# Performance work log

Hardware: AMD Instinct MI355X
Metric: run time of the kernel (lower is better)

The kernel has to match this reference:

```python
import jax, jax.numpy as jnp
import numpy as np

B = 16384
D_VIS, D_LANG, D_STATE = 768, 768, 64
D = 256          # d_model
E = 4            # n_experts
K = 2            # top_k
D_IN = D_VIS + D_LANG + D_STATE
EPS = 1e-5


def layernorm(x, g, b):
    mu = x.mean(-1, keepdims=True)
    var = ((x - mu) ** 2).mean(-1, keepdims=True)
    return g * (x - mu) / jnp.sqrt(var + EPS) + b


def setup_inputs() -> dict:
    key = jax.random.key(0)
    ks = jax.random.split(key, 16)
    s = 0.02
    return {
        "vis": jax.random.normal(ks[0], (B, D_VIS), jnp.float32),
        "lang": jax.random.normal(ks[1], (B, D_LANG), jnp.float32),
        "state": jax.random.normal(ks[2], (B, D_STATE), jnp.float32),
        # fusion: Linear(d_in, d_model) + LayerNorm
        "Wf": jax.random.normal(ks[3], (D_IN, D), jnp.float32) * s,
        "bf": jnp.zeros((D,), jnp.float32),
        "gf": jnp.ones((D,), jnp.float32),
        "bfln": jnp.zeros((D,), jnp.float32),
        # gate (bias=False); random instead of zeros so routing is nontrivial
        "Wg": jax.random.normal(ks[4], (D, E), jnp.float32) * s,
        # stacked experts: Linear(d,2d) -> GELU -> Linear(2d,d) -> GELU -> Linear(d,d), then LN(x + net(x))
        "W1": jax.random.normal(ks[5], (E, D, 2 * D), jnp.float32) * s,
        "b1": jnp.zeros((E, 2 * D), jnp.float32),
        "W2": jax.random.normal(ks[6], (E, 2 * D, D), jnp.float32) * s,
        "b2": jnp.zeros((E, D), jnp.float32),
        "W3": jax.random.normal(ks[7], (E, D, D), jnp.float32) * s,
        "b3": jnp.zeros((E, D), jnp.float32),
        "eg": jnp.ones((E, D), jnp.float32),
        "eb": jnp.zeros((E, D), jnp.float32),
    }


def reference(vis, lang, state, Wf, bf, gf, bfln, Wg, W1, b1, W2, b2, W3, b3, eg, eb):
    gelu = lambda t: jax.nn.gelu(t, approximate=False)
    # fusion: Linear -> LayerNorm -> GELU  (dropout is eval-mode identity)
    x = jnp.concatenate([vis, lang, state], axis=-1) @ Wf + bf   # [B, D]
    x = gelu(layernorm(x, gf, bfln))

    logits = x @ Wg                                              # [B, E]
    all_probs = jax.nn.softmax(logits, axis=-1)
    top_vals, top_idx = jax.lax.top_k(logits, K)                 # [B, K]
    top_w = jax.nn.softmax(top_vals, axis=-1)                    # [B, K]

    # all experts densely (E small); original computes same math per masked subset
    h = gelu(jnp.einsum('bd,edh->beh', x, W1) + b1)              # [B, E, 2D]
    h = gelu(jnp.einsum('beh,ehd->bed', h, W2) + b2)             # [B, E, D]
    h = jnp.einsum('bed,edf->bef', h, W3) + b3                   # [B, E, D]
    y = layernorm(x[:, None, :] + h, eg, eb)                     # [B, E, D]

    # gather selected experts and combine with top-k weights
    y_sel = jnp.take_along_axis(y, top_idx[:, :, None], axis=1)  # [B, K, D]
    out = jnp.einsum('bk,bkd->bd', top_w, y_sel)                 # [B, D]

    # load-balance loss: importance x load
    counts = jnp.zeros((E,), x.dtype).at[top_idx.reshape(-1)].add(1.0)
    f_i = counts / (B * K)
    lb_loss = E * jnp.sum(f_i * all_probs.mean(0))
    return out, lb_loss
```

## Files before the change

### kernel.cpp

```cpp
#include <hip/hip_runtime.h>
#include <math.h>


typedef unsigned short u16;
typedef unsigned int u32;
typedef __attribute__((ext_vector_type(8))) short bf16x8;
typedef __attribute__((ext_vector_type(4))) float f32x4;

__device__ __forceinline__ float bf2f(u16 u) {
    union { u32 i; float f; } v; v.i = ((u32)u) << 16; return v.f;
}
__device__ __forceinline__ u16 f2bf(float f) {
    union { float f; u32 i; } v; v.f = f;
    u32 x = v.i;
    return (u16)((x + 0x7fffu + ((x >> 16) & 1u)) >> 16);
}
__device__ __forceinline__ float gelu_exact(float v) {
    return 0.5f * v * (1.0f + erff(v * 0.70710678118654752f));
}

typedef __attribute__((address_space(1))) void GV;
typedef __attribute__((address_space(3))) void SV;
__device__ __forceinline__ void gldlds(const void* g, void* l) {
    __builtin_amdgcn_global_load_lds((GV*)g, (SV*)l, 16, 0, 0);
}

__device__ __forceinline__ u32 pk2(u32 f0, u32 f1) {
    return __builtin_amdgcn_perm(f1, f0, 0x07060302);
}

__device__ __forceinline__ void stageA64(const u16* Ag, int lda, u16* As, int tid) {
#pragma unroll
    for (int i = 0; i < 2; ++i) {
        int s = i * 256 + tid;
        int m = s >> 3, c = s & 7;
        gldlds(Ag + m * lda + (c ^ (m & 7)) * 8, As + s * 8);
    }
}
__device__ __forceinline__ void stageA64_R32(const u16* Ag, int lda, u16* As, int tid) {
    int s = tid;
    int m = s >> 3, c = s & 7;
    gldlds(Ag + m * lda + (c ^ (m & 7)) * 8, As + s * 8);
}
__device__ __forceinline__ void stageB64(const u16* Bg, int ldb, u16* Bs, int tid) {
#pragma unroll
    for (int i = 0; i < 8; ++i) {
        int s = i * 256 + tid;
        int n = s >> 3, c = s & 7;
        gldlds(Bg + n * ldb + (c ^ (n & 7)) * 8, Bs + s * 8);
    }
}
__device__ __forceinline__ void compute64(const u16* As, const u16* Bs, f32x4 acc[4][4],
                                          int w, int l16, int quad) {
#pragma unroll
    for (int ks = 0; ks < 2; ++ks) {
        bf16x8 a[4];
#pragma unroll
        for (int mt = 0; mt < 4; ++mt) {
            int m = mt * 16 + l16;
            a[mt] = *(const bf16x8*)(As + m * 64 + (((ks * 4 + quad) ^ (m & 7)) << 3));
        }
#pragma unroll
        for (int nt = 0; nt < 4; ++nt) {
            int n = w * 64 + nt * 16 + l16;
            bf16x8 b = *(const bf16x8*)(Bs + n * 64 + (((ks * 4 + quad) ^ (n & 7)) << 3));
#pragma unroll
            for (int mt = 0; mt < 4; ++mt)
                acc[mt][nt] = __builtin_amdgcn_mfma_f32_16x16x32_bf16(a[mt], b, acc[mt][nt], 0, 0, 0);
        }
    }
}
__device__ __forceinline__ void compute64_R32(const u16* As, const u16* Bs, f32x4 acc[2][4],
                                              int w, int l16, int quad) {
#pragma unroll
    for (int ks = 0; ks < 2; ++ks) {
        bf16x8 a[2];
#pragma unroll
        for (int mt = 0; mt < 2; ++mt) {
            int m = mt * 16 + l16;
            a[mt] = *(const bf16x8*)(As + m * 64 + (((ks * 4 + quad) ^ (m & 7)) << 3));
        }
#pragma unroll
        for (int nt = 0; nt < 4; ++nt) {
            int n = w * 64 + nt * 16 + l16;
            bf16x8 b = *(const bf16x8*)(Bs + n * 64 + (((ks * 4 + quad) ^ (n & 7)) << 3));
#pragma unroll
            for (int mt = 0; mt < 2; ++mt)
                acc[mt][nt] = __builtin_amdgcn_mfma_f32_16x16x32_bf16(a[mt], b, acc[mt][nt], 0, 0, 0);
        }
    }
}

#define SEG_WF  409600
#define SEG_W1  524288
#define SEG_W2  524288
#define SEG_W3  262144
#define PREP_ITEMS (SEG_WF + SEG_W1 + SEG_W2 + SEG_W3 + 8)

__global__ __launch_bounds__(256) void prep_kernel(
    const float* __restrict__ Wf, const float* __restrict__ W1, const float* __restrict__ W2,
    const float* __restrict__ W3,
    u16* __restrict__ wft, u16* __restrict__ w1t, u16* __restrict__ w2t, u16* __restrict__ w3t,
    float* __restrict__ lbacc) {
    int idx = blockIdx.x * 256 + threadIdx.x;
    if (idx < SEG_WF) {
        int n = idx / 1600, k = idx % 1600;
        wft[idx] = f2bf(Wf[(size_t)k * 256 + n]);
        return;
    }
    idx -= SEG_WF;
    if (idx < SEG_W1) {
        int e = idx >> 17, r = idx & 131071;
        int n = r >> 8, k = r & 255;
        w1t[idx] = f2bf(W1[(size_t)e * 131072 + (size_t)k * 512 + n]);
        return;
    }
    idx -= SEG_W1;
    if (idx < SEG_W2) {
        int e = idx >> 17, r = idx & 131071;
        int n = r >> 9, k = r & 511;
        w2t[idx] = f2bf(W2[(size_t)e * 131072 + (size_t)k * 256 + n]);
        return;
    }
    idx -= SEG_W2;
    if (idx < SEG_W3) {
        int e = idx >> 16, r = idx & 65535;
        int n = r >> 8, k = r & 255;
        w3t[idx] = f2bf(W3[(size_t)e * 65536 + (size_t)k * 256 + n]);
        return;
    }
    idx -= SEG_W3;
    if (idx < 8) lbacc[idx] = 0.0f;
}

__global__ __launch_bounds__(256) void fusion_kernel(
    const float* __restrict__ vis, const float* __restrict__ lang, const float* __restrict__ state,
    const u16* __restrict__ BT, const float* __restrict__ bfv_, const float* __restrict__ gf,
    const float* __restrict__ bfln, const float* __restrict__ Wg,
    u16* __restrict__ xbf, float* __restrict__ wr, float* __restrict__ lbacc) {
    __shared__ __align__(16) u32 Af[2048];
    __shared__ __align__(16) u16 Bs[16384];
    int tid = threadIdx.x;
    int w = tid >> 6, lane = tid & 63, quad = lane >> 4, l16 = lane & 15;
    int m0 = blockIdx.x * 32;
    f32x4 acc[2][4] = {};

    for (int kit = 0; kit < 25; ++kit) {
        const float* base; int ld;
        if (kit < 12)      { base = vis   + (size_t)m0 * 768 + kit * 64;        ld = 768; }
        else if (kit < 24) { base = lang  + (size_t)m0 * 768 + (kit - 12) * 64; ld = 768; }
        else               { base = state + (size_t)m0 * 64;                    ld = 64; }
#pragma unroll
        for (int i = 0; i < 2; ++i) {
            int s = i * 256 + tid;
            int m = s >> 4, c = s & 15;
            gldlds(base + m * ld + (c ^ (m & 15)) * 4, Af + s * 4);
        }
        stageB64(BT + kit * 64, 1600, Bs, tid);
        __syncthreads();
#pragma unroll
        for (int ks = 0; ks < 2; ++ks) {
            bf16x8 a[2];
#pragma unroll
            for (int mt = 0; mt < 2; ++mt) {
                int m = mt * 16 + l16;
                int c0 = ks * 8 + quad * 2;
                const u32* rowp = Af + m * 64;
                uint4 f0 = *(const uint4*)(rowp + (c0 ^ (m & 15)) * 4);
                uint4 f1 = *(const uint4*)(rowp + ((c0 + 1) ^ (m & 15)) * 4);
                union { u32 u[4]; bf16x8 v; } pk;
                pk.u[0] = pk2(f0.x, f0.y); pk.u[1] = pk2(f0.z, f0.w);
                pk.u[2] = pk2(f1.x, f1.y); pk.u[3] = pk2(f1.z, f1.w);
                a[mt] = pk.v;
            }
#pragma unroll
            for (int nt = 0; nt < 4; ++nt) {
                int n = w * 64 + nt * 16 + l16;
                bf16x8 b = *(const bf16x8*)(Bs + n * 64 + (((ks * 4 + quad) ^ (n & 7)) << 3));
#pragma unroll
                for (int mt = 0; mt < 2; ++mt)
                    acc[mt][nt] = __builtin_amdgcn_mfma_f32_16x16x32_bf16(a[mt], b, acc[mt][nt], 0, 0, 0);
            }
        }
        __syncthreads();
    }

    float2* red  = (float2*)Af;
    float*  muv  = (float*)(Af + 256);
    float*  rsv  = (float*)(Af + 288);
    float*  gred = (float*)(Af + 512);
    float*  sacc = (float*)(Af + 1024);

    float bv[4], gvv[4], blv[4]; float4 wgv[4];
#pragma unroll
    for (int nt = 0; nt < 4; ++nt) {
        int col = w * 64 + nt * 16 + l16;
        bv[nt] = bfv_[col]; gvv[nt] = gf[col]; blv[nt] = bfln[col];
        wgv[nt] = *(const float4*)(Wg + col * 4);
    }
    if (tid < 8) sacc[tid] = 0.f;
#pragma unroll
    for (int mt = 0; mt < 2; ++mt)
#pragma unroll
        for (int r = 0; r < 4; ++r) {
            float ss = 0.f, qq = 0.f;
#pragma unroll
            for (int nt = 0; nt < 4; ++nt) {
                float v = acc[mt][nt][r] + bv[nt];
                acc[mt][nt][r] = v;
                ss += v; qq += v * v;
            }
#pragma unroll
            for (int d = 1; d < 16; d <<= 1) { ss += __shfl_xor(ss, d); qq += __shfl_xor(qq, d); }
            if (l16 == 0) red[w * 32 + mt * 16 + quad * 4 + r] = make_float2(ss, qq);
        }
    __syncthreads();
    if (tid < 32) {
        float ss = 0.f, qq = 0.f;
#pragma unroll
        for (int ww = 0; ww < 4; ++ww) { float2 t = red[ww * 32 + tid]; ss += t.x; qq += t.y; }
        float mu = ss * (1.f / 256.f);
        float var = qq * (1.f / 256.f) - mu * mu;
        muv[tid] = mu;
        rsv[tid] = 1.f / sqrtf(var + 1e-5f);
    }
    __syncthreads();
#pragma unroll
    for (int mt = 0; mt < 2; ++mt)
#pragma unroll
        for (int r = 0; r < 4; ++r) {
            int rl = mt * 16 + quad * 4 + r;
            float mu = muv[rl], rs = rsv[rl];
#pragma unroll
            for (int nt = 0; nt < 4; ++nt) {
                int col = w * 64 + nt * 16 + l16;
                float t = (acc[mt][nt][r] - mu) * rs * gvv[nt] + blv[nt];
                float g = gelu_exact(t);
                acc[mt][nt][r] = g;
                xbf[(size_t)(m0 + rl) * 256 + col] = f2bf(g);
            }
        }
#pragma unroll
    for (int mt = 0; mt < 2; ++mt)
#pragma unroll
        for (int r = 0; r < 4; ++r) {
            int rl = mt * 16 + quad * 4 + r;
            float p0 = 0.f, p1 = 0.f, p2 = 0.f, p3 = 0.f;
#pragma unroll
            for (int nt = 0; nt < 4; ++nt) {
                float g = acc[mt][nt][r];
                p0 += g * wgv[nt].x; p1 += g * wgv[nt].y;
                p2 += g * wgv[nt].z; p3 += g * wgv[nt].w;
            }
#pragma unroll
            for (int d = 1; d < 16; d <<= 1) {
                p0 += __shfl_xor(p0, d); p1 += __shfl_xor(p1, d);
                p2 += __shfl_xor(p2, d); p3 += __shfl_xor(p3, d);
            }
            if (l16 == 0) {
                float* gp = gred + w * 128 + rl * 4;
                gp[0] = p0; gp[1] = p1; gp[2] = p2; gp[3] = p3;
            }
        }
    __syncthreads();
    if (tid < 32) {
        int row = tid;
        float lg[4];
#pragma unroll
        for (int e = 0; e < 4; ++e)
            lg[e] = gred[row * 4 + e] + gred[128 + row * 4 + e] +
                    gred[256 + row * 4 + e] + gred[384 + row * 4 + e];
        float mx = fmaxf(fmaxf(lg[0], lg[1]), fmaxf(lg[2], lg[3]));
        float ex[4]; float Z = 0.f;
#pragma unroll
        for (int e = 0; e < 4; ++e) { ex[e] = expf(lg[e] - mx); Z += ex[e]; }
        int i0 = 0; float v0 = lg[0];
#pragma unroll
        for (int e = 1; e < 4; ++e) if (lg[e] > v0) { v0 = lg[e]; i0 = e; }
        int i1 = -1; float v1 = -1e30f;
#pragma unroll
        for (int e = 0; e < 4; ++e) if (e != i0 && lg[e] > v1) { v1 = lg[e]; i1 = e; }
        float t = expf(v1 - v0);
        float wA = 1.f / (1.f + t), wB = t / (1.f + t);
        float w4[4] = {0.f, 0.f, 0.f, 0.f};
        w4[i0] = wA; w4[i1] = wB;
#pragma unroll
        for (int e = 0; e < 4; ++e) wr[(size_t)(m0 + row) * 4 + e] = w4[e];
#pragma unroll
        for (int e = 0; e < 4; ++e) atomicAdd(&sacc[e], ex[e] / Z);
        atomicAdd(&sacc[4 + i0], 1.f);
        atomicAdd(&sacc[4 + i1], 1.f);
    }
    __syncthreads();
    if (tid < 8) atomicAdd(lbacc + tid, sacc[tid]);
}

__global__ __launch_bounds__(256) void expert_gemm_kernel(
    const u16* __restrict__ A, int lda, size_t aE,
    const u16* __restrict__ BT, size_t bE,
    const float* __restrict__ bias, int biasE,
    u16* __restrict__ outp, int ldo, size_t oE) {
    __shared__ __align__(16) u16 As[4096];
    __shared__ __align__(16) u16 Bs[16384];
    int tid = threadIdx.x;
    int w = tid >> 6, lane = tid & 63, quad = lane >> 4, l16 = lane & 15;
    int m0 = blockIdx.x * 64;
    int col0 = blockIdx.y * 256;
    int e = blockIdx.z;
    f32x4 acc[4][4] = {};
    const u16* Ag = A + e * aE + (size_t)m0 * lda;
    const u16* Bg = BT + e * bE + (size_t)col0 * lda;
    int kiters = lda >> 6;
    for (int kit = 0; kit < kiters; ++kit) {
        stageA64(Ag + kit * 64, lda, As, tid);
        stageB64(Bg + kit * 64, lda, Bs, tid);
        __syncthreads();
        compute64(As, Bs, acc, w, l16, quad);
        __syncthreads();
    }
#pragma unroll
    for (int nt = 0; nt < 4; ++nt) {
        int col = col0 + w * 64 + nt * 16 + l16;
        float bvv = bias[e * biasE + col];
#pragma unroll
        for (int mt = 0; mt < 4; ++mt)
#pragma unroll
            for (int r = 0; r < 4; ++r) {
                int row = m0 + mt * 16 + quad * 4 + r;
                outp[e * oE + (size_t)row * ldo + col] = f2bf(gelu_exact(acc[mt][nt][r] + bvv));
            }
    }
}

__global__ __launch_bounds__(256) void combine_kernel(
    const u16* __restrict__ h2, const u16* __restrict__ W3T,
    const float* __restrict__ b3, const float* __restrict__ eg, const float* __restrict__ eb,
    const u16* __restrict__ xbf, const float* __restrict__ wr,
    const float* __restrict__ lbacc, float* __restrict__ outp) {
    __shared__ __align__(16) u16 As[2048];
    __shared__ __align__(16) u16 Bs[16384];
    __shared__ __align__(16) u16 xs[8192];
    __shared__ float wl[128];
    int tid = threadIdx.x;
    int w = tid >> 6, lane = tid & 63, quad = lane >> 4, l16 = lane & 15;
    int m0 = blockIdx.x * 32;
    if (blockIdx.x == 0 && tid == 0) {
        float lb = 0.f;
#pragma unroll
        for (int e = 0; e < 4; ++e)
            lb += (lbacc[4 + e] / 32768.f) * (lbacc[e] / 16384.f);
        outp[4194304] = 4.f * lb;
    }
#pragma unroll
    for (int i = 0; i < 4; ++i) {
        int s = i * 256 + tid;
        *(uint4*)(xs + s * 8) = *(const uint4*)(xbf + (size_t)m0 * 256 + s * 8);
    }
    if (tid < 128) wl[tid] = wr[(size_t)m0 * 4 + tid];
    float2* red = (float2*)As;
    float* muv = (float*)((char*)As + 1024);
    float* rsv = (float*)((char*)As + 1152);
    f32x4 oacc[2][4] = {};
    for (int e = 0; e < 4; ++e) {
        __syncthreads();
        f32x4 acc[2][4] = {};
        const u16* Ag = h2 + ((size_t)e * 16384 + m0) * 256;
        const u16* Bg = W3T + (size_t)e * 65536;
        for (int kit = 0; kit < 4; ++kit) {
            stageA64_R32(Ag + kit * 64, 256, As, tid);
            stageB64(Bg + kit * 64, 256, Bs, tid);
            __syncthreads();
            compute64_R32(As, Bs, acc, w, l16, quad);
            __syncthreads();
        }
        float b3v[4], egv[4], ebv[4];
#pragma unroll
        for (int nt = 0; nt < 4; ++nt) {
            int col = w * 64 + nt * 16 + l16;
            b3v[nt] = b3[e * 256 + col]; egv[nt] = eg[e * 256 + col]; ebv[nt] = eb[e * 256 + col];
        }
#pragma unroll
        for (int mt = 0; mt < 2; ++mt)
#pragma unroll
            for (int r = 0; r < 4; ++r) {
                int rl = mt * 16 + quad * 4 + r;
                float ss = 0.f, qq = 0.f;
#pragma unroll
                for (int nt = 0; nt < 4; ++nt) {
                    int col = w * 64 + nt * 16 + l16;
                    float v = acc[mt][nt][r] + b3v[nt] + bf2f(xs[rl * 256 + col]);
                    acc[mt][nt][r] = v;
                    ss += v; qq += v * v;
                }
#pragma unroll
                for (int d = 1; d < 16; d <<= 1) { ss += __shfl_xor(ss, d); qq += __shfl_xor(qq, d); }
                if (l16 == 0) red[w * 32 + rl] = make_float2(ss, qq);
            }
        __syncthreads();
        if (tid < 32) {
            float ss = 0.f, qq = 0.f;
#pragma unroll
            for (int ww = 0; ww < 4; ++ww) { float2 t = red[ww * 32 + tid]; ss += t.x; qq += t.y; }
            float mu = ss * (1.f / 256.f);
            float var = qq * (1.f / 256.f) - mu * mu;
            muv[tid] = mu;
            rsv[tid] = 1.f / sqrtf(var + 1e-5f);
        }
        __syncthreads();
#pragma unroll
        for (int mt = 0; mt < 2; ++mt)
#pragma unroll
            for (int r = 0; r < 4; ++r) {
                int rl = mt * 16 + quad * 4 + r;
                float mu = muv[rl], rs = rsv[rl], we = wl[rl * 4 + e];
#pragma unroll
                for (int nt = 0; nt < 4; ++nt) {
                    float y = (acc[mt][nt][r] - mu) * rs * egv[nt] + ebv[nt];
                    oacc[mt][nt][r] += we * y;
                }
            }
    }
#pragma unroll
    for (int mt = 0; mt < 2; ++mt)
#pragma unroll
        for (int r = 0; r < 4; ++r) {
            int rl = mt * 16 + quad * 4 + r;
#pragma unroll
            for (int nt = 0; nt < 4; ++nt) {
                int col = w * 64 + nt * 16 + l16;
                outp[(size_t)(m0 + rl) * 256 + col] = oacc[mt][nt][r];
            }
        }
}

extern "C" void kernel_launch(void* const* d_in, const int* in_sizes, int n_in,
                              void* d_out, int out_size, void* d_ws, size_t ws_size,
                              hipStream_t stream) {
    const float* vis   = (const float*)d_in[0];
    const float* lang  = (const float*)d_in[1];
    const float* state = (const float*)d_in[2];
    const float* Wf    = (const float*)d_in[3];
    const float* bf_   = (const float*)d_in[4];
    const float* gf    = (const float*)d_in[5];
    const float* bfln  = (const float*)d_in[6];
    const float* Wg    = (const float*)d_in[7];
    const float* W1    = (const float*)d_in[8];
    const float* b1    = (const float*)d_in[9];
    const float* W2    = (const float*)d_in[10];
    const float* b2    = (const float*)d_in[11];
    const float* W3    = (const float*)d_in[12];
    const float* b3    = (const float*)d_in[13];
    const float* eg    = (const float*)d_in[14];
    const float* eb    = (const float*)d_in[15];
    float* outp = (float*)d_out;

    char* ws = (char*)d_ws;
    size_t off = 0;
    float* lbacc = (float*)(ws + off); off += 256;
    u16* WFT  = (u16*)(ws + off); off += 819200UL;
    u16* W1T  = (u16*)(ws + off); off += 1048576UL;
    u16* W2T  = (u16*)(ws + off); off += 1048576UL;
    u16* W3T  = (u16*)(ws + off); off += 524288UL;
    u16* XBF  = (u16*)(ws + off); off += 8388608UL;
    float* WR = (float*)(ws + off); off += 262144UL;
    u16* H1   = (u16*)(ws + off); off += 67108864UL;
    u16* H2   = (u16*)(ws + off); off += 33554432UL;
    if (ws_size < off) return;

    int prep_blocks = (PREP_ITEMS + 255) / 256;
    prep_kernel<<<prep_blocks, 256, 0, stream>>>(Wf, W1, W2, W3, WFT, W1T, W2T, W3T, lbacc);
    fusion_kernel<<<512, 256, 0, stream>>>(vis, lang, state, WFT, bf_, gf, bfln, Wg,
                                           XBF, WR, lbacc);
    expert_gemm_kernel<<<dim3(256, 2, 4), 256, 0, stream>>>(
        XBF, 256, 0, W1T, 131072, b1, 512, H1, 512, 8388608UL);
    expert_gemm_kernel<<<dim3(256, 1, 4), 256, 0, stream>>>(
        H1, 512, 8388608UL, W2T, 131072, b2, 256, H2, 256, 4194304UL);
    combine_kernel<<<512, 256, 0, stream>>>(H2, W3T, b3, eg, eb, XBF, WR, lbacc, outp);
}
```

Before: 322.4 us.

## Fuse expert MLP chain into one kernel and stream fusion GEMM via registers

Merges the two expert GEMM kernels and the combine kernel into a single moe_kernel that keeps the H1/H2 intermediates in padded LDS per 32-row tile, so the large global round trips for hidden activations disappear. The fusion GEMM drops LDS staging and instead loads A (fp32) and B tiles straight into registers with a software-pipelined multi-buffer, avoiding barriers. Exact erf GELU is replaced by a tanh-style sigmoid approximation, which changes numerics slightly. Weights are now read directly from global/L2 by each wave, which raises register pressure and may lower occupancy.

```diff
diff --git a/kernel.cpp b/kernel.cpp
--- a/kernel.cpp
+++ b/kernel.cpp
@@ -15,80 +15,12 @@
     u32 x = v.i;
     return (u16)((x + 0x7fffu + ((x >> 16) & 1u)) >> 16);
 }
-__device__ __forceinline__ float gelu_exact(float v) {
-    return 0.5f * v * (1.0f + erff(v * 0.70710678118654752f));
-}
-
-typedef __attribute__((address_space(1))) void GV;
-typedef __attribute__((address_space(3))) void SV;
-__device__ __forceinline__ void gldlds(const void* g, void* l) {
-    __builtin_amdgcn_global_load_lds((GV*)g, (SV*)l, 16, 0, 0);
-}
-
+__device__ __forceinline__ float gelu_fast(float x) {
+    float t = x * (1.59576912f + 0.07135481f * x * x);
+    return x / (1.f + __expf(-t));
+}
 __device__ __forceinline__ u32 pk2(u32 f0, u32 f1) {
     return __builtin_amdgcn_perm(f1, f0, 0x07060302);
-}
-
-__device__ __forceinline__ void stageA64(const u16* Ag, int lda, u16* As, int tid) {
-#pragma unroll
-    for (int i = 0; i < 2; ++i) {
-        int s = i * 256 + tid;
-        int m = s >> 3, c = s & 7;
-        gldlds(Ag + m * lda + (c ^ (m & 7)) * 8, As + s * 8);
-    }
-}
-__device__ __forceinline__ void stageA64_R32(const u16* Ag, int lda, u16* As, int tid) {
-    int s = tid;
-    int m = s >> 3, c = s & 7;
-    gldlds(Ag + m * lda + (c ^ (m & 7)) * 8, As + s * 8);
-}
-__device__ __forceinline__ void stageB64(const u16* Bg, int ldb, u16* Bs, int tid) {
-#pragma unroll
-    for (int i = 0; i < 8; ++i) {
-        int s = i * 256 + tid;
-        int n = s >> 3, c = s & 7;
-        gldlds(Bg + n * ldb + (c ^ (n & 7)) * 8, Bs + s * 8);
-    }
-}
-__device__ __forceinline__ void compute64(const u16* As, const u16* Bs, f32x4 acc[4][4],
-                                          int w, int l16, int quad) {
-#pragma unroll
-    for (int ks = 0; ks < 2; ++ks) {
-        bf16x8 a[4];
-#pragma unroll
-        for (int mt = 0; mt < 4; ++mt) {
-            int m = mt * 16 + l16;
-            a[mt] = *(const bf16x8*)(As + m * 64 + (((ks * 4 + quad) ^ (m & 7)) << 3));
-        }
-#pragma unroll
-        for (int nt = 0; nt < 4; ++nt) {
-            int n = w * 64 + nt * 16 + l16;
-            bf16x8 b = *(const bf16x8*)(Bs + n * 64 + (((ks * 4 + quad) ^ (n & 7)) << 3));
-#pragma unroll
-            for (int mt = 0; mt < 4; ++mt)
-                acc[mt][nt] = __builtin_amdgcn_mfma_f32_16x16x32_bf16(a[mt], b, acc[mt][nt], 0, 0, 0);
-        }
-    }
-}
-__device__ __forceinline__ void compute64_R32(const u16* As, const u16* Bs, f32x4 acc[2][4],
-                                              int w, int l16, int quad) {
-#pragma unroll
-    for (int ks = 0; ks < 2; ++ks) {
-        bf16x8 a[2];
-#pragma unroll
-        for (int mt = 0; mt < 2; ++mt) {
-            int m = mt * 16 + l16;
-            a[mt] = *(const bf16x8*)(As + m * 64 + (((ks * 4 + quad) ^ (m & 7)) << 3));
-        }
-#pragma unroll
-        for (int nt = 0; nt < 4; ++nt) {
-            int n = w * 64 + nt * 16 + l16;
-            bf16x8 b = *(const bf16x8*)(Bs + n * 64 + (((ks * 4 + quad) ^ (n & 7)) << 3));
-#pragma unroll
-            for (int mt = 0; mt < 2; ++mt)
-                acc[mt][nt] = __builtin_amdgcn_mfma_f32_16x16x32_bf16(a[mt], b, acc[mt][nt], 0, 0, 0);
-        }
-    }
 }
 
 #define SEG_WF  409600
@@ -138,58 +70,62 @@
     const u16* __restrict__ BT, const float* __restrict__ bfv_, const float* __restrict__ gf,
     const float* __restrict__ bfln, const float* __restrict__ Wg,
     u16* __restrict__ xbf, float* __restrict__ wr, float* __restrict__ lbacc) {
-    __shared__ __align__(16) u32 Af[2048];
-    __shared__ __align__(16) u16 Bs[16384];
-    int tid = threadIdx.x;
-    int w = tid >> 6, lane = tid & 63, quad = lane >> 4, l16 = lane & 15;
+    __shared__ float2 red[128];
+    __shared__ float muv[32], rsv[32];
+    __shared__ float gred[512];
+    __shared__ float sacc[8];
+    int tid = threadIdx.x, w = tid >> 6, lane = tid & 63, quad = lane >> 4, l16 = lane & 15;
     int m0 = blockIdx.x * 32;
     f32x4 acc[2][4] = {};
-
-    for (int kit = 0; kit < 25; ++kit) {
+    uint4 aR[3][2][2];
+    uint4 bR[2][4];
+
+    auto loadA = [&](int k, int s) {
         const float* base; int ld;
-        if (kit < 12)      { base = vis   + (size_t)m0 * 768 + kit * 64;        ld = 768; }
-        else if (kit < 24) { base = lang  + (size_t)m0 * 768 + (kit - 12) * 64; ld = 768; }
-        else               { base = state + (size_t)m0 * 64;                    ld = 64; }
-#pragma unroll
-        for (int i = 0; i < 2; ++i) {
-            int s = i * 256 + tid;
-            int m = s >> 4, c = s & 15;
-            gldlds(base + m * ld + (c ^ (m & 15)) * 4, Af + s * 4);
-        }
-        stageB64(BT + kit * 64, 1600, Bs, tid);
-        __syncthreads();
-#pragma unroll
-        for (int ks = 0; ks < 2; ++ks) {
-            bf16x8 a[2];
-#pragma unroll
-            for (int mt = 0; mt < 2; ++mt) {
-                int m = mt * 16 + l16;
-                int c0 = ks * 8 + quad * 2;
-                const u32* rowp = Af + m * 64;
-                uint4 f0 = *(const uint4*)(rowp + (c0 ^ (m & 15)) * 4);
-                uint4 f1 = *(const uint4*)(rowp + ((c0 + 1) ^ (m & 15)) * 4);
-                union { u32 u[4]; bf16x8 v; } pk;
-                pk.u[0] = pk2(f0.x, f0.y); pk.u[1] = pk2(f0.z, f0.w);
-                pk.u[2] = pk2(f1.x, f1.y); pk.u[3] = pk2(f1.z, f1.w);
-                a[mt] = pk.v;
-            }
-#pragma unroll
-            for (int nt = 0; nt < 4; ++nt) {
-                int n = w * 64 + nt * 16 + l16;
-                bf16x8 b = *(const bf16x8*)(Bs + n * 64 + (((ks * 4 + quad) ^ (n & 7)) << 3));
-#pragma unroll
-                for (int mt = 0; mt < 2; ++mt)
-                    acc[mt][nt] = __builtin_amdgcn_mfma_f32_16x16x32_bf16(a[mt], b, acc[mt][nt], 0, 0, 0);
-            }
-        }
-        __syncthreads();
-    }
-
-    float2* red  = (float2*)Af;
-    float*  muv  = (float*)(Af + 256);
-    float*  rsv  = (float*)(Af + 288);
-    float*  gred = (float*)(Af + 512);
-    float*  sacc = (float*)(Af + 1024);
+        if (k < 24)      { base = vis + k * 32;          ld = 768; }
+        else if (k < 48) { base = lang + (k - 24) * 32;  ld = 768; }
+        else             { base = state + (k - 48) * 32; ld = 64; }
+#pragma unroll
+        for (int mt = 0; mt < 2; ++mt) {
+            const float* p = base + (size_t)(m0 + mt * 16 + l16) * ld + quad * 8;
+            aR[s][mt][0] = *(const uint4*)p;
+            aR[s][mt][1] = *(const uint4*)(p + 4);
+        }
+    };
+    auto loadB = [&](int k, int s) {
+#pragma unroll
+        for (int nt = 0; nt < 4; ++nt) {
+            int n = w * 64 + nt * 16 + l16;
+            bR[s][nt] = *(const uint4*)(BT + (size_t)n * 1600 + k * 32 + quad * 8);
+        }
+    };
+    auto comp = [&](int sa, int sb) {
+        bf16x8 av[2];
+#pragma unroll
+        for (int mt = 0; mt < 2; ++mt) {
+            union { u32 u[4]; bf16x8 v; } pk;
+            pk.u[0] = pk2(aR[sa][mt][0].x, aR[sa][mt][0].y);
+            pk.u[1] = pk2(aR[sa][mt][0].z, aR[sa][mt][0].w);
+            pk.u[2] = pk2(aR[sa][mt][1].x, aR[sa][mt][1].y);
+            pk.u[3] = pk2(aR[sa][mt][1].z, aR[sa][mt][1].w);
+            av[mt] = pk.v;
+        }
+#pragma unroll
+        for (int nt = 0; nt < 4; ++nt) {
+            union { uint4 u; bf16x8 v; } bb; bb.u = bR[sb][nt];
+#pragma unroll
+            for (int mt = 0; mt < 2; ++mt)
+                acc[mt][nt] = __builtin_amdgcn_mfma_f32_16x16x32_bf16(av[mt], bb.v, acc[mt][nt], 0, 0, 0);
+        }
+    };
+
+    loadA(0, 0); loadA(1, 1); loadB(0, 0);
+#pragma unroll
+    for (int k = 0; k < 50; ++k) {
+        if (k + 2 < 50) loadA(k + 2, (k + 2) % 3);
+        if (k + 1 < 50) loadB(k + 1, (k + 1) & 1);
+        comp(k % 3, k & 1);
+    }
 
     float bv[4], gvv[4], blv[4]; float4 wgv[4];
 #pragma unroll
@@ -235,7 +171,7 @@
             for (int nt = 0; nt < 4; ++nt) {
                 int col = w * 64 + nt * 16 + l16;
                 float t = (acc[mt][nt][r] - mu) * rs * gvv[nt] + blv[nt];
-                float g = gelu_exact(t);
+                float g = gelu_fast(t);
                 acc[mt][nt][r] = g;
                 xbf[(size_t)(m0 + rl) * 256 + col] = f2bf(g);
             }
@@ -295,54 +231,22 @@
     if (tid < 8) atomicAdd(lbacc + tid, sacc[tid]);
 }
 
-__global__ __launch_bounds__(256) void expert_gemm_kernel(
-    const u16* __restrict__ A, int lda, size_t aE,
-    const u16* __restrict__ BT, size_t bE,
-    const float* __restrict__ bias, int biasE,
-    u16* __restrict__ outp, int ldo, size_t oE) {
-    __shared__ __align__(16) u16 As[4096];
-    __shared__ __align__(16) u16 Bs[16384];
-    int tid = threadIdx.x;
-    int w = tid >> 6, lane = tid & 63, quad = lane >> 4, l16 = lane & 15;
-    int m0 = blockIdx.x * 64;
-    int col0 = blockIdx.y * 256;
-    int e = blockIdx.z;
-    f32x4 acc[4][4] = {};
-    const u16* Ag = A + e * aE + (size_t)m0 * lda;
-    const u16* Bg = BT + e * bE + (size_t)col0 * lda;
-    int kiters = lda >> 6;
-    for (int kit = 0; kit < kiters; ++kit) {
-        stageA64(Ag + kit * 64, lda, As, tid);
-        stageB64(Bg + kit * 64, lda, Bs, tid);
-        __syncthreads();
-        compute64(As, Bs, acc, w, l16, quad);
-        __syncthreads();
-    }
-#pragma unroll
-    for (int nt = 0; nt < 4; ++nt) {
-        int col = col0 + w * 64 + nt * 16 + l16;
-        float bvv = bias[e * biasE + col];
-#pragma unroll
-        for (int mt = 0; mt < 4; ++mt)
-#pragma unroll
-            for (int r = 0; r < 4; ++r) {
-                int row = m0 + mt * 16 + quad * 4 + r;
-                outp[e * oE + (size_t)row * ldo + col] = f2bf(gelu_exact(acc[mt][nt][r] + bvv));
-            }
-    }
-}
-
-__global__ __launch_bounds__(256) void combine_kernel(
-    const u16* __restrict__ h2, const u16* __restrict__ W3T,
+#define LDX  264
+#define LDH1 520
+#define LDH2 264
+
+__global__ __launch_bounds__(256) void moe_kernel(
+    const u16* __restrict__ xbf, const u16* __restrict__ W1T, const u16* __restrict__ W2T,
+    const u16* __restrict__ W3T, const float* __restrict__ b1, const float* __restrict__ b2,
     const float* __restrict__ b3, const float* __restrict__ eg, const float* __restrict__ eb,
-    const u16* __restrict__ xbf, const float* __restrict__ wr,
-    const float* __restrict__ lbacc, float* __restrict__ outp) {
-    __shared__ __align__(16) u16 As[2048];
-    __shared__ __align__(16) u16 Bs[16384];
-    __shared__ __align__(16) u16 xs[8192];
+    const float* __restrict__ wr, const float* __restrict__ lbacc, float* __restrict__ outp) {
+    __shared__ __align__(16) u16 xs[32 * LDX];
+    __shared__ __align__(16) u16 h1s[32 * LDH1];
+    __shared__ __align__(16) u16 h2s[32 * LDH2];
     __shared__ float wl[128];
-    int tid = threadIdx.x;
-    int w = tid >> 6, lane = tid & 63, quad = lane >> 4, l16 = lane & 15;
+    __shared__ float2 red[128];
+    __shared__ float muv[32], rsv[32];
+    int tid = threadIdx.x, w = tid >> 6, lane = tid & 63, quad = lane >> 4, l16 = lane & 15;
     int m0 = blockIdx.x * 32;
     if (blockIdx.x == 0 && tid == 0) {
         float lb = 0.f;
@@ -353,72 +257,179 @@
     }
 #pragma unroll
     for (int i = 0; i < 4; ++i) {
-        int s = i * 256 + tid;
-        *(uint4*)(xs + s * 8) = *(const uint4*)(xbf + (size_t)m0 * 256 + s * 8);
+        int s = i * 256 + tid, r = s >> 5, c = s & 31;
+        *(uint4*)(xs + r * LDX + c * 8) = *(const uint4*)(xbf + (size_t)(m0 + r) * 256 + c * 8);
     }
     if (tid < 128) wl[tid] = wr[(size_t)m0 * 4 + tid];
-    float2* red = (float2*)As;
-    float* muv = (float*)((char*)As + 1024);
-    float* rsv = (float*)((char*)As + 1152);
+    __syncthreads();
+
     f32x4 oacc[2][4] = {};
+#pragma unroll 1
     for (int e = 0; e < 4; ++e) {
+        {
+            f32x4 a1[2][8] = {};
+            const u16* Bg = W1T + (size_t)e * 131072 + (size_t)(w * 128) * 256;
+            uint4 bR[2][8];
+#pragma unroll
+            for (int nt = 0; nt < 8; ++nt)
+                bR[0][nt] = *(const uint4*)(Bg + (size_t)(nt * 16 + l16) * 256 + quad * 8);
+#pragma unroll
+            for (int kit = 0; kit < 8; ++kit) {
+                if (kit + 1 < 8) {
+#pragma unroll
+                    for (int nt = 0; nt < 8; ++nt)
+                        bR[(kit + 1) & 1][nt] = *(const uint4*)(Bg + (size_t)(nt * 16 + l16) * 256 + (kit + 1) * 32 + quad * 8);
+                }
+                bf16x8 av[2];
+#pragma unroll
+                for (int mt = 0; mt < 2; ++mt)
+                    av[mt] = *(const bf16x8*)(xs + (mt * 16 + l16) * LDX + kit * 32 + quad * 8);
+#pragma unroll
+                for (int nt = 0; nt < 8; ++nt) {
+                    union { uint4 u; bf16x8 v; } bb; bb.u = bR[kit & 1][nt];
+#pragma unroll
+                    for (int mt = 0; mt < 2; ++mt)
+                        a1[mt][nt] = __builtin_amdgcn_mfma_f32_16x16x32_bf16(av[mt], bb.v, a1[mt][nt], 0, 0, 0);
+                }
+            }
+            __syncthreads();
+            float b1v[8];
+#pragma unroll
+            for (int nt = 0; nt < 8; ++nt) b1v[nt] = b1[e * 512 + w * 128 + nt * 16 + l16];
+#pragma unroll
+            for (int mt = 0; mt < 2; ++mt)
+#pragma unroll
+                for (int nt = 0; nt < 8; ++nt)
+#pragma unroll
+                    for (int r = 0; r < 4; ++r) {
+                        float v = gelu_fast(a1[mt][nt][r] + b1v[nt]);
+                        float o = __shfl_xor(v, 1);
+                        u16 hA = f2bf(v), hB = f2bf(o);
+                        u32 dw = (l16 & 1) ? ((u32)hB | ((u32)hA << 16)) : ((u32)hA | ((u32)hB << 16));
+                        if (!(l16 & 1))
+                            *(u32*)(h1s + (mt * 16 + quad * 4 + r) * LDH1 + w * 128 + nt * 16 + l16) = dw;
+                    }
+        }
         __syncthreads();
-        f32x4 acc[2][4] = {};
-        const u16* Ag = h2 + ((size_t)e * 16384 + m0) * 256;
-        const u16* Bg = W3T + (size_t)e * 65536;
-        for (int kit = 0; kit < 4; ++kit) {
-            stageA64_R32(Ag + kit * 64, 256, As, tid);
-            stageB64(Bg + kit * 64, 256, Bs, tid);
+
+        {
+            f32x4 a2[2][4] = {};
+            const u16* Bg = W2T + (size_t)e * 131072 + (size_t)(w * 64) * 512;
+            uint4 bR[2][4];
+#pragma unroll
+            for (int nt = 0; nt < 4; ++nt)
+                bR[0][nt] = *(const uint4*)(Bg + (size_t)(nt * 16 + l16) * 512 + quad * 8);
+#pragma unroll
+            for (int kit = 0; kit < 16; ++kit) {
+                if (kit + 1 < 16) {
+#pragma unroll
+                    for (int nt = 0; nt < 4; ++nt)
+                        bR[(kit + 1) & 1][nt] = *(const uint4*)(Bg + (size_t)(nt * 16 + l16) * 512 + (kit + 1) * 32 + quad * 8);
+                }
+                bf16x8 av[2];
+#pragma unroll
+                for (int mt = 0; mt < 2; ++mt)
+                    av[mt] = *(const bf16x8*)(h1s + (mt * 16 + l16) * LDH1 + kit * 32 + quad * 8);
+#pragma unroll
+                for (int nt = 0; nt < 4; ++nt) {
+                    union { uint4 u; bf16x8 v; } bb; bb.u = bR[kit & 1][nt];
+#pragma unroll
+                    for (int mt = 0; mt < 2; ++mt)
+                        a2[mt][nt] = __builtin_amdgcn_mfma_f32_16x16x32_bf16(av[mt], bb.v, a2[mt][nt], 0, 0, 0);
+                }
+            }
+            float b2v[4];
+#pragma unroll
+            for (int nt = 0; nt < 4; ++nt) b2v[nt] = b2[e * 256 + w * 64 + nt * 16 + l16];
+#pragma unroll
+            for (int mt = 0; mt < 2; ++mt)
+#pragma unroll
+                for (int nt = 0; nt < 4; ++nt)
+#pragma unroll
+                    for (int r = 0; r < 4; ++r) {
+                        float v = gelu_fast(a2[mt][nt][r] + b2v[nt]);
+                        float o = __shfl_xor(v, 1);
+                        u16 hA = f2bf(v), hB = f2bf(o);
+                        u32 dw = (l16 & 1) ? ((u32)hB | ((u32)hA << 16)) : ((u32)hA | ((u32)hB << 16));
+                        if (!(l16 & 1))
+                            *(u32*)(h2s + (mt * 16 + quad * 4 + r) * LDH2 + w * 64 + nt * 16 + l16) = dw;
+                    }
+        }
+        __syncthreads();
+
+        {
+            f32x4 a3[2][4] = {};
+            const u16* Bg = W3T + (size_t)e * 65536 + (size_t)(w * 64) * 256;
+            uint4 bR[2][4];
+#pragma unroll
+            for (int nt = 0; nt < 4; ++nt)
+                bR[0][nt] = *(const uint4*)(Bg + (size_t)(nt * 16 + l16) * 256 + quad * 8);
+#pragma unroll
+            for (int kit = 0; kit < 8; ++kit) {
+                if (kit + 1 < 8) {
+#pragma unroll
+                    for (int nt = 0; nt < 4; ++nt)
+                        bR[(kit + 1) & 1][nt] = *(const uint4*)(Bg + (size_t)(nt * 16 + l16) * 256 + (kit + 1) * 32 + quad * 8);
+                }
+                bf16x8 av[2];
+#pragma unroll
+                for (int mt = 0; mt < 2; ++mt)
+                    av[mt] = *(const bf16x8*)(h2s + (mt * 16 + l16) * LDH2 + kit * 32 + quad * 8);
+#pragma unroll
+                for (int nt = 0; nt < 4; ++nt) {
+                    union { uint4 u; bf16x8 v; } bb; bb.u = bR[kit & 1][nt];
+#pragma unroll
+                    for (int mt = 0; mt < 2; ++mt)
+                        a3[mt][nt] = __builtin_amdgcn_mfma_f32_16x16x32_bf16(av[mt], bb.v, a3[mt][nt], 0, 0, 0);
+                }
+            }
+            float b3v[4], egv[4], ebv[4];
+#pragma unroll
+            for (int nt = 0; nt < 4; ++nt) {
+                int col = w * 64 + nt * 16 + l16;
+                b3v[nt] = b3[e * 256 + col]; egv[nt] = eg[e * 256 + col]; ebv[nt] = eb[e * 256 + col];
+            }
+#pragma unroll
+            for (int mt = 0; mt < 2; ++mt)
+#pragma unroll
+                for (int r = 0; r < 4; ++r) {
+                    int rl = mt * 16 + quad * 4 + r;
+                    float ss = 0.f, qq = 0.f;
+#pragma unroll
+                    for (int nt = 0; nt < 4; ++nt) {
+                        int col = w * 64 + nt * 16 + l16;
+                        float v = a3[mt][nt][r] + b3v[nt] + bf2f(xs[rl * LDX + col]);
+                        a3[mt][nt][r] = v;
+                        ss += v; qq += v * v;
+                    }
+#pragma unroll
+                    for (int d = 1; d < 16; d <<= 1) { ss += __shfl_xor(ss, d); qq += __shfl_xor(qq, d); }
+                    if (l16 == 0) red[w * 32 + rl] = make_float2(ss, qq);
+                }
             __syncthreads();
-            compute64_R32(As, Bs, acc, w, l16, quad);
+            if (tid < 32) {
+                float ss = 0.f, qq = 0.f;
+#pragma unroll
+                for (int ww = 0; ww < 4; ++ww) { float2 t = red[ww * 32 + tid]; ss += t.x; qq += t.y; }
+                float mu = ss * (1.f / 256.f);
+                float var = qq * (1.f / 256.f) - mu * mu;
+                muv[tid] = mu;
+                rsv[tid] = 1.f / sqrtf(var + 1e-5f);
+            }
             __syncthreads();
-        }
-        float b3v[4], egv[4], ebv[4];
-#pragma unroll
-        for (int nt = 0; nt < 4; ++nt) {
-            int col = w * 64 + nt * 16 + l16;
-            b3v[nt] = b3[e * 256 + col]; egv[nt] = eg[e * 256 + col]; ebv[nt] = eb[e * 256 + col];
-        }
-#pragma unroll
-        for (int mt = 0; mt < 2; ++mt)
-#pragma unroll
-            for (int r = 0; r < 4; ++r) {
-                int rl = mt * 16 + quad * 4 + r;
-                float ss = 0.f, qq = 0.f;
-#pragma unroll
-                for (int nt = 0; nt < 4; ++nt) {
-                    int col = w * 64 + nt * 16 + l16;
-                    float v = acc[mt][nt][r] + b3v[nt] + bf2f(xs[rl * 256 + col]);
-                    acc[mt][nt][r] = v;
-                    ss += v; qq += v * v;
-                }
-#pragma unroll
-                for (int d = 1; d < 16; d <<= 1) { ss += __shfl_xor(ss, d); qq += __shfl_xor(qq, d); }
-                if (l16 == 0) red[w * 32 + rl] = make_float2(ss, qq);
-            }
-        __syncthreads();
-        if (tid < 32) {
-            float ss = 0.f, qq = 0.f;
-#pragma unroll
-            for (int ww = 0; ww < 4; ++ww) { float2 t = red[ww * 32 + tid]; ss += t.x; qq += t.y; }
-            float mu = ss * (1.f / 256.f);
-            float var = qq * (1.f / 256.f) - mu * mu;
-            muv[tid] = mu;
-            rsv[tid] = 1.f / sqrtf(var + 1e-5f);
-        }
-        __syncthreads();
-#pragma unroll
-        for (int mt = 0; mt < 2; ++mt)
-#pragma unroll
-            for (int r = 0; r < 4; ++r) {
-                int rl = mt * 16 + quad * 4 + r;
-                float mu = muv[rl], rs = rsv[rl], we = wl[rl * 4 + e];
-#pragma unroll
-                for (int nt = 0; nt < 4; ++nt) {
-                    float y = (acc[mt][nt][r] - mu) * rs * egv[nt] + ebv[nt];
-                    oacc[mt][nt][r] += we * y;
-                }
-            }
+#pragma unroll
+            for (int mt = 0; mt < 2; ++mt)
+#pragma unroll
+                for (int r = 0; r < 4; ++r) {
+                    int rl = mt * 16 + quad * 4 + r;
+                    float mu = muv[rl], rs = rsv[rl], we = wl[rl * 4 + e];
+#pragma unroll
+                    for (int nt = 0; nt < 4; ++nt) {
+                        float y = (a3[mt][nt][r] - mu) * rs * egv[nt] + ebv[nt];
+                        oacc[mt][nt][r] += we * y;
+                    }
+                }
+        }
     }
 #pragma unroll
     for (int mt = 0; mt < 2; ++mt)
@@ -463,17 +474,12 @@
     u16* W3T  = (u16*)(ws + off); off += 524288UL;
     u16* XBF  = (u16*)(ws + off); off += 8388608UL;
     float* WR = (float*)(ws + off); off += 262144UL;
-    u16* H1   = (u16*)(ws + off); off += 67108864UL;
-    u16* H2   = (u16*)(ws + off); off += 33554432UL;
     if (ws_size < off) return;
 
     int prep_blocks = (PREP_ITEMS + 255) / 256;
     prep_kernel<<<prep_blocks, 256, 0, stream>>>(Wf, W1, W2, W3, WFT, W1T, W2T, W3T, lbacc);
     fusion_kernel<<<512, 256, 0, stream>>>(vis, lang, state, WFT, bf_, gf, bfln, Wg,
                                            XBF, WR, lbacc);
-    expert_gemm_kernel<<<dim3(256, 2, 4), 256, 0, stream>>>(
-        XBF, 256, 0, W1T, 131072, b1, 512, H1, 512, 8388608UL);
-    expert_gemm_kernel<<<dim3(256, 1, 4), 256, 0, stream>>>(
-        H1, 512, 8388608UL, W2T, 131072, b2, 256, H2, 256, 4194304UL);
-    combine_kernel<<<512, 256, 0, stream>>>(H2, W3T, b3, eg, eb, XBF, WR, lbacc, outp);
-}
+    moe_kernel<<<512, 256, 0, stream>>>(XBF, W1T, W2T, W3T, b1, b2, b3, eg, eb,
+                                        WR, lbacc, outp);
+}
```

Result: slower. 514.7 us (+59.7%).
